# Kernel tuning notes

Hardware: AMD Instinct MI355X
Metric: run time of the kernel (lower is better)

Reference implementation:

```python
import jax, jax.numpy as jnp
import numpy as np

B, T, N, I = 64, 12, 307, 3   # batch, timesteps, nodes, input features
R, D = 64, 10                 # rnn_units, embed_dim


def setup_inputs() -> dict:
    key = jax.random.key(0)
    ks = iter(jax.random.split(key, 64))
    def p(*shape):
        return jax.random.normal(next(ks), shape, jnp.float32) * 0.1
    return dict(
        x=jax.random.normal(next(ks), (B, T, N, I), jnp.float32),
        node_emb1=p(N, D), node_emb2=p(N, D),
        # x_embedding MLP: 1 -> 16 -> 2 -> D
        xe_w1=p(16, 1), xe_b1=p(16), xe_w2=p(2, 16), xe_b2=p(2), xe_w3=p(D, 2), xe_b3=p(D),
        # fc1 MLP: I -> 16 -> 2 -> D
        fc1_w1=p(16, I), fc1_b1=p(16), fc1_w2=p(2, 16), fc1_b2=p(2), fc1_w3=p(D, 2), fc1_b3=p(D),
        # fc2 MLP: R -> 16 -> 2 -> D
        fc2_w1=p(16, R), fc2_b1=p(16), fc2_w2=p(2, 16), fc2_b2=p(2), fc2_w3=p(D, 2), fc2_b3=p(D),
        # GRU1 (input D -> hidden R), gates ordered r,z,n as in torch
        gru1_wih=p(3 * R, D), gru1_whh=p(3 * R, R), gru1_bih=p(3 * R), gru1_bhh=p(3 * R),
        # GRU2 (input R -> hidden R)
        gru2_wih=p(3 * R, R), gru2_whh=p(3 * R, R), gru2_bih=p(3 * R), gru2_bhh=p(3 * R),
        weights_pool=p(D, R, R), bias_pool=p(D, R),
        # 1x1 conv == linear over channels: [R, 2R]
        diff_w=p(R, 2 * R), diff_b=p(R),
    )


def _mlp(x, w1, b1, w2, b2, w3, b3):
    h = jax.nn.sigmoid(x @ w1.T + b1)
    h = jax.nn.sigmoid(h @ w2.T + b2)
    return h @ w3.T + b3


def _gru(xs, h0, wih, whh, bih, bhh):
    # xs: [T, B', Din]; torch GRU gate order: r, z, n
    xw = xs @ wih.T + bih  # precompute input projections [T, B', 3R]
    def step(h, xw_t):
        hw = h @ whh.T + bhh
        xr, xz, xn = jnp.split(xw_t, 3, -1)
        hr, hz, hn = jnp.split(hw, 3, -1)
        r = jax.nn.sigmoid(xr + hr)
        z = jax.nn.sigmoid(xz + hz)
        n = jnp.tanh(xn + r * hn)
        h = (1.0 - z) * n + z * h
        return h, h
    _, out = jax.lax.scan(step, h0, xw)
    return out  # [T, B', R]


def reference(x, node_emb1, node_emb2,
              xe_w1, xe_b1, xe_w2, xe_b2, xe_w3, xe_b3,
              fc1_w1, fc1_b1, fc1_w2, fc1_b2, fc1_w3, fc1_b3,
              fc2_w1, fc2_b1, fc2_w2, fc2_b2, fc2_w3, fc2_b3,
              gru1_wih, gru1_whh, gru1_bih, gru1_bhh,
              gru2_wih, gru2_whh, gru2_bih, gru2_bhh,
              weights_pool, bias_pool, diff_w, diff_b):
    # --- feature-level dynamic dependency ---
    node_embed = _mlp(x[..., None], xe_w1, xe_b1, xe_w2, xe_b2, xe_w3, xe_b3)  # [B,T,N,I,D]
    supports_node2 = jax.nn.relu(jnp.einsum('btnjd,btnid->btnji', node_embed, node_embed))  # [B,T,N,I,I]
    # x1 = eye(I) @ x == x (identity support kept implicit)
    x2 = jnp.einsum('btnji,btni->btnj', supports_node2, x)
    input_for_fc1 = x + x2
    g1_in = _mlp(input_for_fc1, fc1_w1, fc1_b1, fc1_w2, fc1_b2, fc1_w3, fc1_b3)  # [B,T,N,D]
    g1_in = jnp.transpose(g1_in, (1, 0, 2, 3)).reshape(T, B * N, D)
    h0 = jnp.zeros((B * N, R), jnp.float32)
    out1 = _gru(g1_in, h0, gru1_wih, gru1_whh, gru1_bih, gru1_bhh).reshape(T, B, N, R)
    # --- node-level dynamic dependency ---
    filt = _mlp(out1, fc2_w1, fc2_b1, fc2_w2, fc2_b2, fc2_w3, fc2_b3)  # [T,B,N,D]
    nodevec = jnp.tanh(node_emb1 * filt)  # broadcast [N,D] over [T,B,N,D]
    supports2 = jax.nn.relu(jnp.einsum('tbnd,tbmd->tbnm', nodevec, nodevec))  # [T,B,N,N]
    # x_g1 = eye(N) @ out1 == out1
    x_g = out1 + jnp.einsum('tbnm,tbmc->tbnc', supports2, out1)
    weights = jnp.einsum('nd,dcr->ncr', node_emb2, weights_pool)  # [N,R,R]
    bias = node_emb2 @ bias_pool                                   # [N,R]
    diff1 = jnp.einsum('tbnc,ncr->tbnr', x_g, weights) + bias      # [T,B,N,R]
    # --- 1x1 conv over channels + GRU2 (dropout in eval mode: identity) ---
    cat = jnp.concatenate([out1, diff1], axis=-1)                  # [T,B,N,2R]
    g2_in = jnp.einsum('tbnc,rc->tbnr', cat, diff_w) + diff_b      # [T,B,N,R]
    out2 = _gru(g2_in.reshape(T, B * N, R), h0, gru2_wih, gru2_whh, gru2_bih, gru2_bhh)
    return jnp.transpose(out2.reshape(T, B, N, R), (1, 0, 2, 3))   # [B,T,N,R]
```

## Files before the change

kernel.cpp:

```cpp
#include <hip/hip_runtime.h>
#include <hip/hip_fp16.h>
#include <math.h>

#define B_ 64
#define T_ 12
#define N_ 307
#define I_ 3
#define R_ 64
#define D_ 10
#define M_ (B_*N_)
#define TM_ (T_*M_)

typedef _Float16 f16x8 __attribute__((ext_vector_type(8)));
typedef float f32x4 __attribute__((ext_vector_type(4)));

__device__ __forceinline__ float sigm(float x){ return 1.f/(1.f+__expf(-x)); }

__device__ __forceinline__ unsigned pkh(float a, float b){
  unsigned r;
  asm("v_cvt_pkrtz_f16_f32 %0, %1, %2" : "=v"(r) : "v"(a), "v"(b));
  return r;
}

__global__ __launch_bounds__(256) void k_stageA(
    const float* __restrict__ x,
    const float* __restrict__ xw1, const float* __restrict__ xb1,
    const float* __restrict__ xw2, const float* __restrict__ xb2,
    const float* __restrict__ xw3, const float* __restrict__ xb3,
    const float* __restrict__ fw1, const float* __restrict__ fb1,
    const float* __restrict__ fw2, const float* __restrict__ fb2,
    const float* __restrict__ fw3, const float* __restrict__ fb3,
    float* __restrict__ g1)
{
  int idx = blockIdx.x*256 + threadIdx.x;
  int t = idx / M_;
  int m = idx - t*M_;
  int b = m / N_;
  int n = m - b*N_;
  const float* xp = x + (((size_t)b*T_ + t)*N_ + n)*I_;
  float xv[3] = {xp[0], xp[1], xp[2]};
  float e[3][10];
  #pragma unroll
  for (int i=0;i<3;++i){
    float h1[16];
    #pragma unroll
    for (int u=0;u<16;++u) h1[u] = sigm(xv[i]*xw1[u] + xb1[u]);
    float h2[2];
    #pragma unroll
    for (int v=0;v<2;++v){
      float a = xb2[v];
      #pragma unroll
      for (int u=0;u<16;++u) a += h1[u]*xw2[v*16+u];
      h2[v] = sigm(a);
    }
    #pragma unroll
    for (int d=0;d<10;++d) e[i][d] = xb3[d] + h2[0]*xw3[d*2] + h2[1]*xw3[d*2+1];
  }
  float in1[3];
  #pragma unroll
  for (int j=0;j<3;++j){
    float acc = 0.f;
    #pragma unroll
    for (int i=0;i<3;++i){
      float s = 0.f;
      #pragma unroll
      for (int d=0;d<10;++d) s += e[j][d]*e[i][d];
      s = fmaxf(s, 0.f);
      acc += s*xv[i];
    }
    in1[j] = xv[j] + acc;
  }
  float h1[16];
  #pragma unroll
  for (int u=0;u<16;++u)
    h1[u] = sigm(fb1[u] + in1[0]*fw1[u*3] + in1[1]*fw1[u*3+1] + in1[2]*fw1[u*3+2]);
  float h2[2];
  #pragma unroll
  for (int v=0;v<2;++v){
    float a = fb2[v];
    #pragma unroll
    for (int u=0;u<16;++u) a += h1[u]*fw2[v*16+u];
    h2[v] = sigm(a);
  }
  float* gp = g1 + (size_t)idx*10;
  #pragma unroll
  for (int d=0;d<10;++d) gp[d] = fb3[d] + h2[0]*fw3[d*2] + h2[1]*fw3[d*2+1];
}

__global__ __launch_bounds__(256) void k_prep(
    const float* __restrict__ wpool, const float* __restrict__ bpool,
    const float* __restrict__ dw,
    float* __restrict__ Wp2, float* __restrict__ bp2)
{
  int d = blockIdx.x; int tid = threadIdx.x;
  __shared__ float WpS[64*68];
  __shared__ float dwBT[64*68];
  __shared__ float bp_s[64];
  for (int idx = tid; idx < 4096; idx += 256) {
    int c = idx >> 6, r = idx & 63;
    WpS[c*68 + r] = wpool[(size_t)d*4096 + idx];
  }
  for (int idx = tid; idx < 4096; idx += 256) {
    int u = idx >> 6, r = idx & 63;
    dwBT[r*68 + u] = dw[u*128 + 64 + r];
  }
  if (tid < 64) bp_s[tid] = bpool[d*64 + tid];
  __syncthreads();
  int u = tid & 63, cg = tid >> 6;
  #pragma unroll
  for (int j = 0; j < 16; ++j) {
    int c = cg*16 + j;
    float acc = 0.f;
    #pragma unroll 8
    for (int r = 0; r < 64; ++r) acc += WpS[c*68 + r] * dwBT[r*68 + u];
    Wp2[(size_t)d*4096 + u*64 + c] = acc;
  }
  if (tid < 64) {
    float acc = 0.f;
    #pragma unroll 8
    for (int r = 0; r < 64; ++r) acc += bp_s[r] * dwBT[r*68 + tid];
    bp2[d*64 + tid] = acc;
  }
}

__global__ __launch_bounds__(256) void k_wnf(
    const float* __restrict__ emb2, const float* __restrict__ Wp2,
    const float* __restrict__ bp2, const float* __restrict__ db,
    float* __restrict__ Wf, float* __restrict__ bf)
{
  int n = blockIdx.x; int tid = threadIdx.x;
  __shared__ float e_s[10];
  if (tid < 10) e_s[tid] = emb2[n*10 + tid];
  __syncthreads();
  #pragma unroll
  for (int e=0;e<16;++e){
    int i = e*256 + tid;
    float a = 0.f;
    #pragma unroll
    for (int d=0;d<10;++d) a += e_s[d]*Wp2[(size_t)d*4096 + i];
    Wf[(size_t)n*4096 + i] = a;
  }
  if (tid < 64){
    float a = db[tid];
    #pragma unroll
    for (int d=0;d<10;++d) a += e_s[d]*bp2[d*64 + tid];
    bf[n*64 + tid] = a;
  }
}

__global__ __launch_bounds__(256) void k_wpackM(
    const float* __restrict__ wih2, const float* __restrict__ whh2,
    const float* __restrict__ wih1, const float* __restrict__ whh1,
    unsigned* __restrict__ Wh2, unsigned* __restrict__ Wx2,
    unsigned* __restrict__ Wh1, unsigned* __restrict__ Wx1)
{
  int i = blockIdx.x*256 + threadIdx.x;
  if (i < 192*32) {
    int wr = i >> 5, p = i & 31;
    Wh2[i] = pkh(whh2[wr*64 + 2*p], whh2[wr*64 + 2*p + 1]);
    Wx2[i] = pkh(wih2[wr*64 + 2*p], wih2[wr*64 + 2*p + 1]);
    Wh1[i] = pkh(whh1[wr*64 + 2*p], whh1[wr*64 + 2*p + 1]);
  }
  int j = i - 192*32;
  if (j >= 0 && j < 192*16) {
    int wr = j >> 4, p = j & 15;
    Wx1[j] = (p < 5) ? pkh(wih1[wr*10 + 2*p], wih1[wr*10 + 2*p + 1]) : 0u;
  }
}

template<int DIN, bool WFIN>
__global__ __launch_bounds__(256, 3) void k_gruM(
    const float* __restrict__ xseq,
    const unsigned* __restrict__ Whf,
    const unsigned* __restrict__ Wxf,
    const float* __restrict__ bih, const float* __restrict__ bhh,
    float* __restrict__ o_out)
{
  constexpr int XPR = (DIN == 64) ? 32 : 16;
  constexpr int XKS = XPR / 16;
  constexpr int XST = XPR + 4;
  __shared__ __align__(16) unsigned Ah_s[16*36];
  __shared__ __align__(16) unsigned Ax_s[16*XST];
  const int tid = threadIdx.x;
  const int lane = tid & 63, w = tid >> 6;
  const int fr = lane & 15, fq = lane >> 4;
  const int row0 = blockIdx.x * 16;
  const int u = w*16 + fr;

  f16x8 bh_r[2], bh_z[2], bh_n[2];
  #pragma unroll
  for (int ks = 0; ks < 2; ++ks) {
    bh_r[ks] = *(const f16x8*)&Whf[(size_t)u*32        + ks*16 + fq*4];
    bh_z[ks] = *(const f16x8*)&Whf[(size_t)(64+u)*32   + ks*16 + fq*4];
    bh_n[ks] = *(const f16x8*)&Whf[(size_t)(128+u)*32  + ks*16 + fq*4];
  }
  f16x8 bx_r[XKS], bx_z[XKS], bx_n[XKS];
  #pragma unroll
  for (int ks = 0; ks < XKS; ++ks) {
    bx_r[ks] = *(const f16x8*)&Wxf[(size_t)u*XPR       + ks*16 + fq*4];
    bx_z[ks] = *(const f16x8*)&Wxf[(size_t)(64+u)*XPR  + ks*16 + fq*4];
    bx_n[ks] = *(const f16x8*)&Wxf[(size_t)(128+u)*XPR + ks*16 + fq*4];
  }

  const float brc = bih[u]     + bhh[u];
  const float bzc = bih[64+u]  + bhh[64+u];
  const float bxn = bih[128+u];
  const float bhn = bhh[128+u];

  for (int i = tid; i < 16*36;  i += 256) Ah_s[i] = 0u;
  for (int i = tid; i < 16*XST; i += 256) Ax_s[i] = 0u;
  __syncthreads();

  size_t obase[4];
  #pragma unroll
  for (int reg = 0; reg < 4; ++reg) {
    int g = row0 + fq*4 + reg;
    if (WFIN) { int bb = g / N_, nn = g - bb*N_; obase[reg] = (((size_t)bb*T_)*N_ + nn)*64 + u; }
    else      { obase[reg] = (size_t)g*64 + u; }
  }
  const size_t tstep = WFIN ? (size_t)N_*64 : (size_t)M_*64;
  float hreg[4] = {0.f, 0.f, 0.f, 0.f};

  for (int t = 0; t < T_; ++t) {
    if (DIN == 64) {
      #pragma unroll
      for (int it = 0; it < 2; ++it) {
        int idx = tid + it*256;
        int row = idx >> 5, p = idx & 31;
        const float2 v = *(const float2*)&xseq[((size_t)t*M_ + row0 + row)*64 + 2*p];
        Ax_s[row*XST + p] = pkh(v.x, v.y);
      }
    } else {
      if (tid < 80) {
        int row = tid / 5, p = tid - (tid/5)*5;
        const float2 v = *(const float2*)&xseq[((size_t)t*M_ + row0 + row)*10 + 2*p];
        Ax_s[row*XST + p] = pkh(v.x, v.y);
      }
    }
    __syncthreads();

    f32x4 ar  = {0.f,0.f,0.f,0.f}, az  = {0.f,0.f,0.f,0.f};
    f32x4 anh = {0.f,0.f,0.f,0.f}, anx = {0.f,0.f,0.f,0.f};
    #pragma unroll
    for (int ks = 0; ks < 2; ++ks) {
      f16x8 ah = *(const f16x8*)&Ah_s[fr*36 + ks*16 + fq*4];
      ar  = __builtin_amdgcn_mfma_f32_16x16x32_f16(ah, bh_r[ks], ar,  0,0,0);
      az  = __builtin_amdgcn_mfma_f32_16x16x32_f16(ah, bh_z[ks], az,  0,0,0);
      anh = __builtin_amdgcn_mfma_f32_16x16x32_f16(ah, bh_n[ks], anh, 0,0,0);
    }
    #pragma unroll
    for (int ks = 0; ks < XKS; ++ks) {
      f16x8 ax = *(const f16x8*)&Ax_s[fr*XST + ks*16 + fq*4];
      ar  = __builtin_amdgcn_mfma_f32_16x16x32_f16(ax, bx_r[ks], ar,  0,0,0);
      az  = __builtin_amdgcn_mfma_f32_16x16x32_f16(ax, bx_z[ks], az,  0,0,0);
      anx = __builtin_amdgcn_mfma_f32_16x16x32_f16(ax, bx_n[ks], anx, 0,0,0);
    }

    float o_new[4];
    #pragma unroll
    for (int reg = 0; reg < 4; ++reg) {
      float rg = sigm(ar[reg] + brc);
      float zg = sigm(az[reg] + bzc);
      float ng = tanhf(anx[reg] + bxn + rg*(anh[reg] + bhn));
      o_new[reg] = (1.f - zg)*ng + zg*hreg[reg];
      hreg[reg] = o_new[reg];
    }
    #pragma unroll
    for (int reg = 0; reg < 4; ++reg)
      o_out[obase[reg] + (size_t)t*tstep] = o_new[reg];

    unsigned pk[4];
    #pragma unroll
    for (int reg = 0; reg < 4; ++reg) {
      float pr = __shfl_xor(o_new[reg], 1);
      pk[reg] = pkh(o_new[reg], pr);
    }
    __syncthreads();
    if ((fr & 1) == 0) {
      #pragma unroll
      for (int reg = 0; reg < 4; ++reg)
        Ah_s[(fq*4 + reg)*36 + w*8 + (fr >> 1)] = pk[reg];
    }
  }
}

__global__ __launch_bounds__(256) void k_stageC(
    const float* __restrict__ out1, const float* __restrict__ emb1,
    const float* __restrict__ w1, const float* __restrict__ b1,
    const float* __restrict__ w2, const float* __restrict__ b2,
    const float* __restrict__ w3, const float* __restrict__ b3,
    float* __restrict__ ndv)
{
  int idx = blockIdx.x*256 + threadIdx.x;
  int m = idx % M_;
  int n = m % N_;
  float rv[64];
  const float4* r4 = (const float4*)(out1 + (size_t)idx*64);
  #pragma unroll
  for (int q=0;q<16;++q){ float4 v=r4[q]; rv[q*4]=v.x; rv[q*4+1]=v.y; rv[q*4+2]=v.z; rv[q*4+3]=v.w; }
  float h1[16];
  for (int u=0;u<16;++u){
    float a = b1[u];
    const float* wr = w1 + u*64;
    #pragma unroll
    for (int c=0;c<64;++c) a += rv[c]*wr[c];
    h1[u] = sigm(a);
  }
  float h2[2];
  #pragma unroll
  for (int v=0;v<2;++v){
    float a = b2[v];
    #pragma unroll
    for (int u=0;u<16;++u) a += h1[u]*w2[v*16+u];
    h2[v] = sigm(a);
  }
  #pragma unroll
  for (int d=0;d<10;++d){
    float f = b3[d] + h2[0]*w3[d*2] + h2[1]*w3[d*2+1];
    ndv[(size_t)idx*10 + d] = tanhf(emb1[n*10+d]*f);
  }
}

__global__ __launch_bounds__(256, 3) void k_stageDM(
    const float* __restrict__ ndv, const float* __restrict__ out1, float* __restrict__ xg)
{
  const int tb = blockIdx.x;
  const int tid = threadIdx.x;
  const int lane = tid & 63, wid = tid >> 6;
  const int fr = lane & 15, fq = lane >> 4;

  __shared__ __align__(16) unsigned Vp_s[320*20];
  __shared__ __align__(16) unsigned P_s[64*36];
  __shared__ __align__(16) unsigned O_s[2][64*36];

  for (int i = tid; i < 320*20; i += 256) {
    int nn = i / 20, p = i - (i/20)*20;
    float a = 0.f, b = 0.f;
    if (nn < N_ && p < 5) {
      const float2 v = *(const float2*)&ndv[((size_t)tb*N_ + nn)*10 + 2*p];
      a = v.x; b = v.y;
    }
    Vp_s[i] = pkh(a, b);
  }

  const float* ob = out1 + (size_t)tb*N_*64;

  for (int it = tid; it < 512; it += 256) {
    int p = it & 31, cg = it >> 5;
    int m0 = 2*p;
    float4 a = make_float4(0.f,0.f,0.f,0.f), b = a;
    if (m0     < N_) a = *(const float4*)&ob[(size_t)m0*64 + cg*4];
    if (m0 + 1 < N_) b = *(const float4*)&ob[(size_t)(m0+1)*64 + cg*4];
    int c0 = cg*4;
    O_s[0][(c0+0)*36 + p] = pkh(a.x, b.x);
    O_s[0][(c0+1)*36 + p] = pkh(a.y, b.y);
    O_s[0][(c0+2)*36 + p] = pkh(a.z, b.z);
    O_s[0][(c0+3)*36 + p] = pkh(a.w, b.w);
  }
  __syncthreads();

  f32x4 acc[5][4];
  #pragma unroll
  for (int a = 0; a < 5; ++a)
    #pragma unroll
    for (int c = 0; c < 4; ++c)
      acc[a][c] = (f32x4){0.f, 0.f, 0.f, 0.f};

  for (int k = 0; k < 5; ++k) {
    const int cur = k & 1;
    const int mc = k*64;
    if (k < 4) {
      int mcn = mc + 64;
      for (int it = tid; it < 512; it += 256) {
        int p = it & 31, cg = it >> 5;
        int m0 = mcn + 2*p;
        float4 a = make_float4(0.f,0.f,0.f,0.f), b = a;
        if (m0     < N_) a = *(const float4*)&ob[(size_t)m0*64 + cg*4];
        if (m0 + 1 < N_) b = *(const float4*)&ob[(size_t)(m0+1)*64 + cg*4];
        int c0 = cg*4;
        O_s[cur^1][(c0+0)*36 + p] = pkh(a.x, b.x);
        O_s[cur^1][(c0+1)*36 + p] = pkh(a.y, b.y);
        O_s[cur^1][(c0+2)*36 + p] = pkh(a.z, b.z);
        O_s[cur^1][(c0+3)*36 + p] = pkh(a.w, b.w);
      }
    }
    f16x8 va[4];
    #pragma unroll
    for (int mt = 0; mt < 4; ++mt)
      va[mt] = *(const f16x8*)&Vp_s[(mc + mt*16 + fr)*20 + fq*4];
    f16x8 bo[2][4];
    #pragma unroll
    for (int ks = 0; ks < 2; ++ks)
      #pragma unroll
      for (int ct = 0; ct < 4; ++ct)
        bo[ks][ct] = *(const f16x8*)&O_s[cur][(ct*16 + fr)*36 + ks*16 + fq*4];

    #pragma unroll
    for (int j = 0; j < 5; ++j) {
      int nt = wid + 4*j;
      f16x8 vb = *(const f16x8*)&Vp_s[(nt*16 + fr)*20 + fq*4];
      #pragma unroll
      for (int mt = 0; mt < 4; ++mt) {
        f32x4 s = (f32x4){0.f,0.f,0.f,0.f};
        s = __builtin_amdgcn_mfma_f32_16x16x32_f16(va[mt], vb, s, 0, 0, 0);
        unsigned p0 = pkh(fmaxf(s[0],0.f), fmaxf(s[1],0.f));
        unsigned p1 = pkh(fmaxf(s[2],0.f), fmaxf(s[3],0.f));
        *(uint2*)&P_s[(wid*16 + fr)*36 + mt*8 + fq*2] = make_uint2(p0, p1);
      }
      #pragma unroll
      for (int ks = 0; ks < 2; ++ks) {
        f16x8 af = *(const f16x8*)&P_s[(wid*16 + fr)*36 + ks*16 + fq*4];
        #pragma unroll
        for (int ct = 0; ct < 4; ++ct)
          acc[j][ct] = __builtin_amdgcn_mfma_f32_16x16x32_f16(af, bo[ks][ct], acc[j][ct], 0, 0, 0);
      }
    }
    __syncthreads();
  }

  #pragma unroll
  for (int j = 0; j < 5; ++j) {
    #pragma unroll
    for (int ct = 0; ct < 4; ++ct) {
      int col = ct*16 + fr;
      #pragma unroll
      for (int reg = 0; reg < 4; ++reg) {
        int n = (wid + 4*j)*16 + fq*4 + reg;
        if (n < N_) {
          size_t base = (size_t)tb*N_*64 + (size_t)n*64 + col;
          xg[base] = out1[base] + acc[j][ct][reg];
        }
      }
    }
  }
}

__global__ __launch_bounds__(256) void k_stageEM(
    const float* xg_in, const float* __restrict__ out1,
    const float* __restrict__ Wf, const float* __restrict__ dw,
    const float* __restrict__ bf,
    float* xg_out)
{
  int n = blockIdx.y;
  int tile = blockIdx.x;
  const int tid = threadIdx.x;
  const int lane = tid & 63, w = tid >> 6;
  const int fr = lane & 15, fq = lane >> 4;
  __shared__ __align__(16) unsigned As[64*68];
  __shared__ __align__(16) unsigned Bs[64*68];
  __shared__ float bf_s[64];

  for (int idx = tid; idx < 1024; idx += 256) {
    int row = idx >> 4, c4 = idx & 15;
    size_t g = ((size_t)(tile*64 + row)*N_ + n)*64 + c4*4;
    float4 o  = *(const float4*)&out1[g];
    float4 xv = *(const float4*)&xg_in[g];
    As[row*68 + c4*2]          = pkh(o.x, o.y);
    As[row*68 + c4*2 + 1]      = pkh(o.z, o.w);
    As[row*68 + 32 + c4*2]     = pkh(xv.x, xv.y);
    As[row*68 + 32 + c4*2 + 1] = pkh(xv.z, xv.w);
    int u = row;
    float4 da = *(const float4*)&dw[u*128 + c4*4];
    float4 wf = *(const float4*)&Wf[(size_t)n*4096 + u*64 + c4*4];
    Bs[u*68 + c4*2]          = pkh(da.x, da.y);
    Bs[u*68 + c4*2 + 1]      = pkh(da.z, da.w);
    Bs[u*68 + 32 + c4*2]     = pkh(wf.x, wf.y);
    Bs[u*68 + 32 + c4*2 + 1] = pkh(wf.z, wf.w);
  }
  if (tid < 64) bf_s[tid] = bf[n*64 + tid];
  __syncthreads();

  f32x4 acc[4];
  #pragma unroll
  for (int ct = 0; ct < 4; ++ct) acc[ct] = (f32x4){0.f,0.f,0.f,0.f};

  #pragma unroll
  for (int ks = 0; ks < 4; ++ks) {
    f16x8 af = *(const f16x8*)&As[(w*16 + fr)*68 + ks*16 + fq*4];
    #pragma unroll
    for (int ct = 0; ct < 4; ++ct) {
      f16x8 bfr = *(const f16x8*)&Bs[(ct*16 + fr)*68 + ks*16 + fq*4];
      acc[ct] = __builtin_amdgcn_mfma_f32_16x16x32_f16(af, bfr, acc[ct], 0, 0, 0);
    }
  }

  #pragma unroll
  for (int ct = 0; ct < 4; ++ct) {
    int u = ct*16 + fr;
    float bfv = bf_s[u];
    #pragma unroll
    for (int reg = 0; reg < 4; ++reg) {
      int row = w*16 + fq*4 + reg;
      xg_out[((size_t)(tile*64 + row)*N_ + n)*64 + u] = acc[ct][reg] + bfv;
    }
  }
}

extern "C" void kernel_launch(void* const* d_in, const int* in_sizes, int n_in,
                              void* d_out, int out_size, void* d_ws, size_t ws_size,
                              hipStream_t stream)
{
  (void)in_sizes; (void)n_in; (void)out_size;
  const float* x    = (const float*)d_in[0];
  const float* emb1 = (const float*)d_in[1];
  const float* emb2 = (const float*)d_in[2];
  const float* xw1  = (const float*)d_in[3];
  const float* xb1  = (const float*)d_in[4];
  const float* xw2  = (const float*)d_in[5];
  const float* xb2  = (const float*)d_in[6];
  const float* xw3  = (const float*)d_in[7];
  const float* xb3  = (const float*)d_in[8];
  const float* fw1  = (const float*)d_in[9];
  const float* fb1  = (const float*)d_in[10];
  const float* fw2  = (const float*)d_in[11];
  const float* fb2  = (const float*)d_in[12];
  const float* fw3  = (const float*)d_in[13];
  const float* fb3  = (const float*)d_in[14];
  const float* c2w1 = (const float*)d_in[15];
  const float* c2b1 = (const float*)d_in[16];
  const float* c2w2 = (const float*)d_in[17];
  const float* c2b2 = (const float*)d_in[18];
  const float* c2w3 = (const float*)d_in[19];
  const float* c2b3 = (const float*)d_in[20];
  const float* g1wih= (const float*)d_in[21];
  const float* g1whh= (const float*)d_in[22];
  const float* g1bih= (const float*)d_in[23];
  const float* g1bhh= (const float*)d_in[24];
  const float* g2wih= (const float*)d_in[25];
  const float* g2whh= (const float*)d_in[26];
  const float* g2bih= (const float*)d_in[27];
  const float* g2bhh= (const float*)d_in[28];
  const float* wpool= (const float*)d_in[29];
  const float* bpool= (const float*)d_in[30];
  const float* dww  = (const float*)d_in[31];
  const float* dwb  = (const float*)d_in[32];
  float* out = (float*)d_out;

  float* ws = (float*)d_ws;
  float* g1_in = ws;
  float* out1  = g1_in + (size_t)TM_*10;
  float* ndv   = out1 + (size_t)TM_*64;
  float* xg    = ndv + (size_t)TM_*10;
  float* Wf    = xg + (size_t)TM_*64;
  float* bf    = Wf + (size_t)N_*4096;
  float* Wp2   = bf + (size_t)N_*64;
  float* bp2   = Wp2 + 10*4096;
  unsigned* Wh2f = (unsigned*)(bp2 + 10*64);
  unsigned* Wx2f = Wh2f + 192*32;
  unsigned* Wh1f = Wx2f + 192*32;
  unsigned* Wx1f = Wh1f + 192*32;
  size_t need = ((size_t)((char*)(Wx1f + 192*16) - (char*)ws));
  if (ws_size < need) return;

  k_stageA<<<TM_/256, 256, 0, stream>>>(x, xw1,xb1,xw2,xb2,xw3,xb3, fw1,fb1,fw2,fb2,fw3,fb3, g1_in);
  k_prep<<<10, 256, 0, stream>>>(wpool, bpool, dww, Wp2, bp2);
  k_wnf<<<N_, 256, 0, stream>>>(emb2, Wp2, bp2, dwb, Wf, bf);
  k_wpackM<<<(192*32 + 192*16 + 255)/256, 256, 0, stream>>>(
      g2wih, g2whh, g1wih, g1whh, Wh2f, Wx2f, Wh1f, Wx1f);

  k_gruM<10,false><<<M_/16, 256, 0, stream>>>(g1_in, Wh1f, Wx1f, g1bih, g1bhh, out1);

  k_stageC<<<TM_/256, 256, 0, stream>>>(out1, emb1, c2w1,c2b1,c2w2,c2b2,c2w3,c2b3, ndv);
  k_stageDM<<<T_*B_, 256, 0, stream>>>(ndv, out1, xg);
  k_stageEM<<<dim3(12, N_), 256, 0, stream>>>(xg, out1, Wf, dww, bf, xg);

  k_gruM<64,true><<<M_/16, 256, 0, stream>>>(xg, Wh2f, Wx2f, g2bih, g2bhh, out);
}
```

Before: 226.2 us.

## Fuse input MLP stage into GRU1 kernel and widen GRU blocks to 32 rows

The per-element input MLP and embedding-attention stage is computed inside the first GRU kernel for all 12 timesteps up front, and the result is stored as packed fp16 in shared memory. This removes the g1_in global write/read round trip and one kernel launch. Both GRU kernels now use 512-thread blocks covering 32 rows (two 16-row groups), which halves the grid and shares weight fragment loads per block. In exchange, more shared memory is used per block, and only 384 of 512 threads do the MLP prologue.

Result: slower. 238.8 us, median of 2 (+5.5%).

```diff
diff --git a/kernel.cpp b/kernel.cpp
--- a/kernel.cpp
+++ b/kernel.cpp
@@ -22,7 +22,88 @@
   return r;
 }
 
-__global__ __launch_bounds__(256) void k_stageA(
+__global__ __launch_bounds__(256) void k_prep(
+    const float* __restrict__ wpool, const float* __restrict__ bpool,
+    const float* __restrict__ dw,
+    float* __restrict__ Wp2, float* __restrict__ bp2)
+{
+  int d = blockIdx.x; int tid = threadIdx.x;
+  __shared__ float WpS[64*68];
+  __shared__ float dwBT[64*68];
+  __shared__ float bp_s[64];
+  for (int idx = tid; idx < 4096; idx += 256) {
+    int c = idx >> 6, r = idx & 63;
+    WpS[c*68 + r] = wpool[(size_t)d*4096 + idx];
+  }
+  for (int idx = tid; idx < 4096; idx += 256) {
+    int u = idx >> 6, r = idx & 63;
+    dwBT[r*68 + u] = dw[u*128 + 64 + r];
+  }
+  if (tid < 64) bp_s[tid] = bpool[d*64 + tid];
+  __syncthreads();
+  int u = tid & 63, cg = tid >> 6;
+  #pragma unroll
+  for (int j = 0; j < 16; ++j) {
+    int c = cg*16 + j;
+    float acc = 0.f;
+    #pragma unroll 8
+    for (int r = 0; r < 64; ++r) acc += WpS[c*68 + r] * dwBT[r*68 + u];
+    Wp2[(size_t)d*4096 + u*64 + c] = acc;
+  }
+  if (tid < 64) {
+    float acc = 0.f;
+    #pragma unroll 8
+    for (int r = 0; r < 64; ++r) acc += bp_s[r] * dwBT[r*68 + tid];
+    bp2[d*64 + tid] = acc;
+  }
+}
+
+__global__ __launch_bounds__(256) void k_wnf(
+    const float* __restrict__ emb2, const float* __restrict__ Wp2,
+    const float* __restrict__ bp2, const float* __restrict__ db,
+    float* __restrict__ Wf, float* __restrict__ bf)
+{
+  int n = blockIdx.x; int tid = threadIdx.x;
+  __shared__ float e_s[10];
+  if (tid < 10) e_s[tid] = emb2[n*10 + tid];
+  __syncthreads();
+  #pragma unroll
+  for (int e=0;e<16;++e){
+    int i = e*256 + tid;
+    float a = 0.f;
+    #pragma unroll
+    for (int d=0;d<10;++d) a += e_s[d]*Wp2[(size_t)d*4096 + i];
+    Wf[(size_t)n*4096 + i] = a;
+  }
+  if (tid < 64){
+    float a = db[tid];
+    #pragma unroll
+    for (int d=0;d<10;++d) a += e_s[d]*bp2[d*64 + tid];
+    bf[n*64 + tid] = a;
+  }
+}
+
+__global__ __launch_bounds__(256) void k_wpackM(
+    const float* __restrict__ wih2, const float* __restrict__ whh2,
+    const float* __restrict__ wih1, const float* __restrict__ whh1,
+    unsigned* __restrict__ Wh2, unsigned* __restrict__ Wx2,
+    unsigned* __restrict__ Wh1, unsigned* __restrict__ Wx1)
+{
+  int i = blockIdx.x*256 + threadIdx.x;
+  if (i < 192*32) {
+    int wr = i >> 5, p = i & 31;
+    Wh2[i] = pkh(whh2[wr*64 + 2*p], whh2[wr*64 + 2*p + 1]);
+    Wx2[i] = pkh(wih2[wr*64 + 2*p], wih2[wr*64 + 2*p + 1]);
+    Wh1[i] = pkh(whh1[wr*64 + 2*p], whh1[wr*64 + 2*p + 1]);
+  }
+  int j = i - 192*32;
+  if (j >= 0 && j < 192*16) {
+    int wr = j >> 4, p = j & 15;
+    Wx1[j] = (p < 5) ? pkh(wih1[wr*10 + 2*p], wih1[wr*10 + 2*p + 1]) : 0u;
+  }
+}
+
+__global__ __launch_bounds__(512, 4) void k_gru1F(
     const float* __restrict__ x,
     const float* __restrict__ xw1, const float* __restrict__ xb1,
     const float* __restrict__ xw2, const float* __restrict__ xb2,
@@ -30,162 +111,19 @@
     const float* __restrict__ fw1, const float* __restrict__ fb1,
     const float* __restrict__ fw2, const float* __restrict__ fb2,
     const float* __restrict__ fw3, const float* __restrict__ fb3,
-    float* __restrict__ g1)
-{
-  int idx = blockIdx.x*256 + threadIdx.x;
-  int t = idx / M_;
-  int m = idx - t*M_;
-  int b = m / N_;
-  int n = m - b*N_;
-  const float* xp = x + (((size_t)b*T_ + t)*N_ + n)*I_;
-  float xv[3] = {xp[0], xp[1], xp[2]};
-  float e[3][10];
-  #pragma unroll
-  for (int i=0;i<3;++i){
-    float h1[16];
-    #pragma unroll
-    for (int u=0;u<16;++u) h1[u] = sigm(xv[i]*xw1[u] + xb1[u]);
-    float h2[2];
-    #pragma unroll
-    for (int v=0;v<2;++v){
-      float a = xb2[v];
-      #pragma unroll
-      for (int u=0;u<16;++u) a += h1[u]*xw2[v*16+u];
-      h2[v] = sigm(a);
-    }
-    #pragma unroll
-    for (int d=0;d<10;++d) e[i][d] = xb3[d] + h2[0]*xw3[d*2] + h2[1]*xw3[d*2+1];
-  }
-  float in1[3];
-  #pragma unroll
-  for (int j=0;j<3;++j){
-    float acc = 0.f;
-    #pragma unroll
-    for (int i=0;i<3;++i){
-      float s = 0.f;
-      #pragma unroll
-      for (int d=0;d<10;++d) s += e[j][d]*e[i][d];
-      s = fmaxf(s, 0.f);
-      acc += s*xv[i];
-    }
-    in1[j] = xv[j] + acc;
-  }
-  float h1[16];
-  #pragma unroll
-  for (int u=0;u<16;++u)
-    h1[u] = sigm(fb1[u] + in1[0]*fw1[u*3] + in1[1]*fw1[u*3+1] + in1[2]*fw1[u*3+2]);
-  float h2[2];
-  #pragma unroll
-  for (int v=0;v<2;++v){
-    float a = fb2[v];
-    #pragma unroll
-    for (int u=0;u<16;++u) a += h1[u]*fw2[v*16+u];
-    h2[v] = sigm(a);
-  }
-  float* gp = g1 + (size_t)idx*10;
-  #pragma unroll
-  for (int d=0;d<10;++d) gp[d] = fb3[d] + h2[0]*fw3[d*2] + h2[1]*fw3[d*2+1];
-}
-
-__global__ __launch_bounds__(256) void k_prep(
-    const float* __restrict__ wpool, const float* __restrict__ bpool,
-    const float* __restrict__ dw,
-    float* __restrict__ Wp2, float* __restrict__ bp2)
-{
-  int d = blockIdx.x; int tid = threadIdx.x;
-  __shared__ float WpS[64*68];
-  __shared__ float dwBT[64*68];
-  __shared__ float bp_s[64];
-  for (int idx = tid; idx < 4096; idx += 256) {
-    int c = idx >> 6, r = idx & 63;
-    WpS[c*68 + r] = wpool[(size_t)d*4096 + idx];
-  }
-  for (int idx = tid; idx < 4096; idx += 256) {
-    int u = idx >> 6, r = idx & 63;
-    dwBT[r*68 + u] = dw[u*128 + 64 + r];
-  }
-  if (tid < 64) bp_s[tid] = bpool[d*64 + tid];
-  __syncthreads();
-  int u = tid & 63, cg = tid >> 6;
-  #pragma unroll
-  for (int j = 0; j < 16; ++j) {
-    int c = cg*16 + j;
-    float acc = 0.f;
-    #pragma unroll 8
-    for (int r = 0; r < 64; ++r) acc += WpS[c*68 + r] * dwBT[r*68 + u];
-    Wp2[(size_t)d*4096 + u*64 + c] = acc;
-  }
-  if (tid < 64) {
-    float acc = 0.f;
-    #pragma unroll 8
-    for (int r = 0; r < 64; ++r) acc += bp_s[r] * dwBT[r*68 + tid];
-    bp2[d*64 + tid] = acc;
-  }
-}
-
-__global__ __launch_bounds__(256) void k_wnf(
-    const float* __restrict__ emb2, const float* __restrict__ Wp2,
-    const float* __restrict__ bp2, const float* __restrict__ db,
-    float* __restrict__ Wf, float* __restrict__ bf)
-{
-  int n = blockIdx.x; int tid = threadIdx.x;
-  __shared__ float e_s[10];
-  if (tid < 10) e_s[tid] = emb2[n*10 + tid];
-  __syncthreads();
-  #pragma unroll
-  for (int e=0;e<16;++e){
-    int i = e*256 + tid;
-    float a = 0.f;
-    #pragma unroll
-    for (int d=0;d<10;++d) a += e_s[d]*Wp2[(size_t)d*4096 + i];
-    Wf[(size_t)n*4096 + i] = a;
-  }
-  if (tid < 64){
-    float a = db[tid];
-    #pragma unroll
-    for (int d=0;d<10;++d) a += e_s[d]*bp2[d*64 + tid];
-    bf[n*64 + tid] = a;
-  }
-}
-
-__global__ __launch_bounds__(256) void k_wpackM(
-    const float* __restrict__ wih2, const float* __restrict__ whh2,
-    const float* __restrict__ wih1, const float* __restrict__ whh1,
-    unsigned* __restrict__ Wh2, unsigned* __restrict__ Wx2,
-    unsigned* __restrict__ Wh1, unsigned* __restrict__ Wx1)
-{
-  int i = blockIdx.x*256 + threadIdx.x;
-  if (i < 192*32) {
-    int wr = i >> 5, p = i & 31;
-    Wh2[i] = pkh(whh2[wr*64 + 2*p], whh2[wr*64 + 2*p + 1]);
-    Wx2[i] = pkh(wih2[wr*64 + 2*p], wih2[wr*64 + 2*p + 1]);
-    Wh1[i] = pkh(whh1[wr*64 + 2*p], whh1[wr*64 + 2*p + 1]);
-  }
-  int j = i - 192*32;
-  if (j >= 0 && j < 192*16) {
-    int wr = j >> 4, p = j & 15;
-    Wx1[j] = (p < 5) ? pkh(wih1[wr*10 + 2*p], wih1[wr*10 + 2*p + 1]) : 0u;
-  }
-}
-
-template<int DIN, bool WFIN>
-__global__ __launch_bounds__(256, 3) void k_gruM(
-    const float* __restrict__ xseq,
     const unsigned* __restrict__ Whf,
     const unsigned* __restrict__ Wxf,
     const float* __restrict__ bih, const float* __restrict__ bhh,
     float* __restrict__ o_out)
 {
-  constexpr int XPR = (DIN == 64) ? 32 : 16;
-  constexpr int XKS = XPR / 16;
-  constexpr int XST = XPR + 4;
-  __shared__ __align__(16) unsigned Ah_s[16*36];
-  __shared__ __align__(16) unsigned Ax_s[16*XST];
+  __shared__ __align__(16) unsigned Ah_s[32*36];
+  __shared__ __align__(16) unsigned Axa_s[12*32*20];
   const int tid = threadIdx.x;
   const int lane = tid & 63, w = tid >> 6;
+  const int g = w >> 2, wl = w & 3;
   const int fr = lane & 15, fq = lane >> 4;
-  const int row0 = blockIdx.x * 16;
-  const int u = w*16 + fr;
+  const int row0 = blockIdx.x * 32;
+  const int u = wl*16 + fr;
 
   f16x8 bh_r[2], bh_z[2], bh_n[2];
   #pragma unroll
@@ -194,66 +132,100 @@
     bh_z[ks] = *(const f16x8*)&Whf[(size_t)(64+u)*32   + ks*16 + fq*4];
     bh_n[ks] = *(const f16x8*)&Whf[(size_t)(128+u)*32  + ks*16 + fq*4];
   }
-  f16x8 bx_r[XKS], bx_z[XKS], bx_n[XKS];
-  #pragma unroll
-  for (int ks = 0; ks < XKS; ++ks) {
-    bx_r[ks] = *(const f16x8*)&Wxf[(size_t)u*XPR       + ks*16 + fq*4];
-    bx_z[ks] = *(const f16x8*)&Wxf[(size_t)(64+u)*XPR  + ks*16 + fq*4];
-    bx_n[ks] = *(const f16x8*)&Wxf[(size_t)(128+u)*XPR + ks*16 + fq*4];
-  }
+  f16x8 bx_r = *(const f16x8*)&Wxf[(size_t)u*16       + fq*4];
+  f16x8 bx_z = *(const f16x8*)&Wxf[(size_t)(64+u)*16  + fq*4];
+  f16x8 bx_n = *(const f16x8*)&Wxf[(size_t)(128+u)*16 + fq*4];
 
   const float brc = bih[u]     + bhh[u];
   const float bzc = bih[64+u]  + bhh[64+u];
   const float bxn = bih[128+u];
   const float bhn = bhh[128+u];
 
-  for (int i = tid; i < 16*36;  i += 256) Ah_s[i] = 0u;
-  for (int i = tid; i < 16*XST; i += 256) Ax_s[i] = 0u;
+  for (int i = tid; i < 32*36;    i += 512) Ah_s[i]  = 0u;
+  for (int i = tid; i < 12*32*20; i += 512) Axa_s[i] = 0u;
   __syncthreads();
 
+  if (tid < 384) {
+    int tt = tid >> 5, row = tid & 31;
+    int m = row0 + row;
+    int b = m / N_, n = m - b*N_;
+    const float* xp = x + (((size_t)b*T_ + tt)*N_ + n)*I_;
+    float xv[3] = {xp[0], xp[1], xp[2]};
+    float e[3][10];
+    #pragma unroll
+    for (int i=0;i<3;++i){
+      float h1[16];
+      #pragma unroll
+      for (int uu=0;uu<16;++uu) h1[uu] = sigm(xv[i]*xw1[uu] + xb1[uu]);
+      float h2[2];
+      #pragma unroll
+      for (int v=0;v<2;++v){
+        float a = xb2[v];
+        #pragma unroll
+        for (int uu=0;uu<16;++uu) a += h1[uu]*xw2[v*16+uu];
+        h2[v] = sigm(a);
+      }
+      #pragma unroll
+      for (int d=0;d<10;++d) e[i][d] = xb3[d] + h2[0]*xw3[d*2] + h2[1]*xw3[d*2+1];
+    }
+    float in1[3];
+    #pragma unroll
+    for (int j=0;j<3;++j){
+      float acc = 0.f;
+      #pragma unroll
+      for (int i=0;i<3;++i){
+        float s = 0.f;
+        #pragma unroll
+        for (int d=0;d<10;++d) s += e[j][d]*e[i][d];
+        s = fmaxf(s, 0.f);
+        acc += s*xv[i];
+      }
+      in1[j] = xv[j] + acc;
+    }
+    float h1[16];
+    #pragma unroll
+    for (int uu=0;uu<16;++uu)
+      h1[uu] = sigm(fb1[uu] + in1[0]*fw1[uu*3] + in1[1]*fw1[uu*3+1] + in1[2]*fw1[uu*3+2]);
+    float h2[2];
+    #pragma unroll
+    for (int v=0;v<2;++v){
+      float a = fb2[v];
+      #pragma unroll
+      for (int uu=0;uu<16;++uu) a += h1[uu]*fw2[v*16+uu];
+      h2[v] = sigm(a);
+    }
+    float gl[10];
+    #pragma unroll
+    for (int d=0;d<10;++d) gl[d] = fb3[d] + h2[0]*fw3[d*2] + h2[1]*fw3[d*2+1];
+    unsigned* ax = &Axa_s[(tt*32 + row)*20];
+    #pragma unroll
+    for (int p=0;p<5;++p) ax[p] = pkh(gl[2*p], gl[2*p+1]);
+  }
+  __syncthreads();
+
   size_t obase[4];
   #pragma unroll
   for (int reg = 0; reg < 4; ++reg) {
-    int g = row0 + fq*4 + reg;
-    if (WFIN) { int bb = g / N_, nn = g - bb*N_; obase[reg] = (((size_t)bb*T_)*N_ + nn)*64 + u; }
-    else      { obase[reg] = (size_t)g*64 + u; }
-  }
-  const size_t tstep = WFIN ? (size_t)N_*64 : (size_t)M_*64;
+    int grow = row0 + g*16 + fq*4 + reg;
+    obase[reg] = (size_t)grow*64 + u;
+  }
   float hreg[4] = {0.f, 0.f, 0.f, 0.f};
 
   for (int t = 0; t < T_; ++t) {
-    if (DIN == 64) {
-      #pragma unroll
-      for (int it = 0; it < 2; ++it) {
-        int idx = tid + it*256;
-        int row = idx >> 5, p = idx & 31;
-        const float2 v = *(const float2*)&xseq[((size_t)t*M_ + row0 + row)*64 + 2*p];
-        Ax_s[row*XST + p] = pkh(v.x, v.y);
-      }
-    } else {
-      if (tid < 80) {
-        int row = tid / 5, p = tid - (tid/5)*5;
-        const float2 v = *(const float2*)&xseq[((size_t)t*M_ + row0 + row)*10 + 2*p];
-        Ax_s[row*XST + p] = pkh(v.x, v.y);
-      }
-    }
-    __syncthreads();
-
     f32x4 ar  = {0.f,0.f,0.f,0.f}, az  = {0.f,0.f,0.f,0.f};
     f32x4 anh = {0.f,0.f,0.f,0.f}, anx = {0.f,0.f,0.f,0.f};
     #pragma unroll
     for (int ks = 0; ks < 2; ++ks) {
-      f16x8 ah = *(const f16x8*)&Ah_s[fr*36 + ks*16 + fq*4];
+      f16x8 ah = *(const f16x8*)&Ah_s[(g*16 + fr)*36 + ks*16 + fq*4];
       ar  = __builtin_amdgcn_mfma_f32_16x16x32_f16(ah, bh_r[ks], ar,  0,0,0);
       az  = __builtin_amdgcn_mfma_f32_16x16x32_f16(ah, bh_z[ks], az,  0,0,0);
       anh = __builtin_amdgcn_mfma_f32_16x16x32_f16(ah, bh_n[ks], anh, 0,0,0);
     }
-    #pragma unroll
-    for (int ks = 0; ks < XKS; ++ks) {
-      f16x8 ax = *(const f16x8*)&Ax_s[fr*XST + ks*16 + fq*4];
-      ar  = __builtin_amdgcn_mfma_f32_16x16x32_f16(ax, bx_r[ks], ar,  0,0,0);
-      az  = __builtin_amdgcn_mfma_f32_16x16x32_f16(ax, bx_z[ks], az,  0,0,0);
-      anx = __builtin_amdgcn_mfma_f32_16x16x32_f16(ax, bx_n[ks], anx, 0,0,0);
+    {
+      f16x8 ax = *(const f16x8*)&Axa_s[(t*32 + g*16 + fr)*20 + fq*4];
+      ar  = __builtin_amdgcn_mfma_f32_16x16x32_f16(ax, bx_r, ar,  0,0,0);
+      az  = __builtin_amdgcn_mfma_f32_16x16x32_f16(ax, bx_z, az,  0,0,0);
+      anx = __builtin_amdgcn_mfma_f32_16x16x32_f16(ax, bx_n, anx, 0,0,0);
     }
 
     float o_new[4];
@@ -267,7 +239,7 @@
     }
     #pragma unroll
     for (int reg = 0; reg < 4; ++reg)
-      o_out[obase[reg] + (size_t)t*tstep] = o_new[reg];
+      o_out[(size_t)t*M_*64 + obase[reg]] = o_new[reg];
 
     unsigned pk[4];
     #pragma unroll
@@ -279,7 +251,103 @@
     if ((fr & 1) == 0) {
       #pragma unroll
       for (int reg = 0; reg < 4; ++reg)
-        Ah_s[(fq*4 + reg)*36 + w*8 + (fr >> 1)] = pk[reg];
+        Ah_s[(g*16 + fq*4 + reg)*36 + wl*8 + (fr >> 1)] = pk[reg];
+    }
+    __syncthreads();
+  }
+}
+
+__global__ __launch_bounds__(512, 4) void k_gru2M(
+    const float* __restrict__ xseq,
+    const unsigned* __restrict__ Whf,
+    const unsigned* __restrict__ Wxf,
+    const float* __restrict__ bih, const float* __restrict__ bhh,
+    float* __restrict__ ofin)
+{
+  __shared__ __align__(16) unsigned Ah_s[32*36];
+  __shared__ __align__(16) unsigned Ax_s[32*36];
+  const int tid = threadIdx.x;
+  const int lane = tid & 63, w = tid >> 6;
+  const int g = w >> 2, wl = w & 3;
+  const int fr = lane & 15, fq = lane >> 4;
+  const int row0 = blockIdx.x * 32;
+  const int u = wl*16 + fr;
+
+  f16x8 bh_r[2], bh_z[2], bh_n[2], bx_r[2], bx_z[2], bx_n[2];
+  #pragma unroll
+  for (int ks = 0; ks < 2; ++ks) {
+    bh_r[ks] = *(const f16x8*)&Whf[(size_t)u*32        + ks*16 + fq*4];
+    bh_z[ks] = *(const f16x8*)&Whf[(size_t)(64+u)*32   + ks*16 + fq*4];
+    bh_n[ks] = *(const f16x8*)&Whf[(size_t)(128+u)*32  + ks*16 + fq*4];
+    bx_r[ks] = *(const f16x8*)&Wxf[(size_t)u*32        + ks*16 + fq*4];
+    bx_z[ks] = *(const f16x8*)&Wxf[(size_t)(64+u)*32   + ks*16 + fq*4];
+    bx_n[ks] = *(const f16x8*)&Wxf[(size_t)(128+u)*32  + ks*16 + fq*4];
+  }
+
+  const float brc = bih[u]     + bhh[u];
+  const float bzc = bih[64+u]  + bhh[64+u];
+  const float bxn = bih[128+u];
+  const float bhn = bhh[128+u];
+
+  for (int i = tid; i < 32*36; i += 512) Ah_s[i] = 0u;
+
+  size_t obase[4];
+  #pragma unroll
+  for (int reg = 0; reg < 4; ++reg) {
+    int grow = row0 + g*16 + fq*4 + reg;
+    int bb = grow / N_, nn = grow - bb*N_;
+    obase[reg] = (((size_t)bb*T_)*N_ + nn)*64 + u;
+  }
+  float hreg[4] = {0.f, 0.f, 0.f, 0.f};
+
+  for (int t = 0; t < T_; ++t) {
+    #pragma unroll
+    for (int it = 0; it < 2; ++it) {
+      int idx = tid + it*512;
+      int row = idx >> 5, p = idx & 31;
+      const float2 v = *(const float2*)&xseq[((size_t)t*M_ + row0 + row)*64 + 2*p];
+      Ax_s[row*36 + p] = pkh(v.x, v.y);
+    }
+    __syncthreads();
+
+    f32x4 ar  = {0.f,0.f,0.f,0.f}, az  = {0.f,0.f,0.f,0.f};
+    f32x4 anh = {0.f,0.f,0.f,0.f}, anx = {0.f,0.f,0.f,0.f};
+    #pragma unroll
+    for (int ks = 0; ks < 2; ++ks) {
+      f16x8 ah = *(const f16x8*)&Ah_s[(g*16 + fr)*36 + ks*16 + fq*4];
+      ar  = __builtin_amdgcn_mfma_f32_16x16x32_f16(ah, bh_r[ks], ar,  0,0,0);
+      az  = __builtin_amdgcn_mfma_f32_16x16x32_f16(ah, bh_z[ks], az,  0,0,0);
+      anh = __builtin_amdgcn_mfma_f32_16x16x32_f16(ah, bh_n[ks], anh, 0,0,0);
+      f16x8 ax = *(const f16x8*)&Ax_s[(g*16 + fr)*36 + ks*16 + fq*4];
+      ar  = __builtin_amdgcn_mfma_f32_16x16x32_f16(ax, bx_r[ks], ar,  0,0,0);
+      az  = __builtin_amdgcn_mfma_f32_16x16x32_f16(ax, bx_z[ks], az,  0,0,0);
+      anx = __builtin_amdgcn_mfma_f32_16x16x32_f16(ax, bx_n[ks], anx, 0,0,0);
+    }
+
+    float o_new[4];
+    #pragma unroll
+    for (int reg = 0; reg < 4; ++reg) {
+      float rg = sigm(ar[reg] + brc);
+      float zg = sigm(az[reg] + bzc);
+      float ng = tanhf(anx[reg] + bxn + rg*(anh[reg] + bhn));
+      o_new[reg] = (1.f - zg)*ng + zg*hreg[reg];
+      hreg[reg] = o_new[reg];
+    }
+    #pragma unroll
+    for (int reg = 0; reg < 4; ++reg)
+      ofin[obase[reg] + (size_t)t*N_*64] = o_new[reg];
+
+    unsigned pk[4];
+    #pragma unroll
+    for (int reg = 0; reg < 4; ++reg) {
+      float pr = __shfl_xor(o_new[reg], 1);
+      pk[reg] = pkh(o_new[reg], pr);
+    }
+    __syncthreads();
+    if ((fr & 1) == 0) {
+      #pragma unroll
+      for (int reg = 0; reg < 4; ++reg)
+        Ah_s[(g*16 + fq*4 + reg)*36 + wl*8 + (fr >> 1)] = pk[reg];
     }
   }
 }
@@ -537,8 +605,7 @@
   float* out = (float*)d_out;
 
   float* ws = (float*)d_ws;
-  float* g1_in = ws;
-  float* out1  = g1_in + (size_t)TM_*10;
+  float* out1  = ws;
   float* ndv   = out1 + (size_t)TM_*64;
   float* xg    = ndv + (size_t)TM_*10;
   float* Wf    = xg + (size_t)TM_*64;
@@ -552,17 +619,18 @@
   size_t need = ((size_t)((char*)(Wx1f + 192*16) - (char*)ws));
   if (ws_size < need) return;
 
-  k_stageA<<<TM_/256, 256, 0, stream>>>(x, xw1,xb1,xw2,xb2,xw3,xb3, fw1,fb1,fw2,fb2,fw3,fb3, g1_in);
   k_prep<<<10, 256, 0, stream>>>(wpool, bpool, dww, Wp2, bp2);
   k_wnf<<<N_, 256, 0, stream>>>(emb2, Wp2, bp2, dwb, Wf, bf);
   k_wpackM<<<(192*32 + 192*16 + 255)/256, 256, 0, stream>>>(
       g2wih, g2whh, g1wih, g1whh, Wh2f, Wx2f, Wh1f, Wx1f);
 
-  k_gruM<10,false><<<M_/16, 256, 0, stream>>>(g1_in, Wh1f, Wx1f, g1bih, g1bhh, out1);
+  k_gru1F<<<M_/32, 512, 0, stream>>>(
+      x, xw1,xb1,xw2,xb2,xw3,xb3, fw1,fb1,fw2,fb2,fw3,fb3,
+      Wh1f, Wx1f, g1bih, g1bhh, out1);
 
   k_stageC<<<TM_/256, 256, 0, stream>>>(out1, emb1, c2w1,c2b1,c2w2,c2b2,c2w3,c2b3, ndv);
   k_stageDM<<<T_*B_, 256, 0, stream>>>(ndv, out1, xg);
   k_stageEM<<<dim3(12, N_), 256, 0, stream>>>(xg, out1, Wf, dww, bf, xg);
 
-  k_gruM<64,true><<<M_/16, 256, 0, stream>>>(xg, Wh2f, Wx2f, g2bih, g2bhh, out);
-}
+  k_gru2M<<<M_/32, 512, 0, stream>>>(xg, Wh2f, Wx2f, g2bih, g2bhh, out);
+}
```
